# Optimization experiments

Hardware: AMD Instinct MI355X
Metric: run time of the kernel (lower is better)

Reference implementation:

```python
import jax, jax.numpy as jnp
import numpy as np

N = 100000   # nodes
G = 128      # graphs for mean pool


def gcn_conv(x, edge_index, W, b, num_nodes):
    # PyG GCNConv (default): x' = D^-1/2 (A+I) D^-1/2 (x W) + b
    x = x @ W
    src, dst = edge_index[0], edge_index[1]
    loop = jnp.arange(num_nodes)
    src = jnp.concatenate([src, loop])
    dst = jnp.concatenate([dst, loop])
    ones = jnp.ones(src.shape[0], x.dtype)
    deg = jax.ops.segment_sum(ones, dst, num_segments=num_nodes)
    dinv = jnp.where(deg > 0, jax.lax.rsqrt(deg), 0.0)
    norm = dinv[src] * dinv[dst]            # [E+N]
    msg = x[src] * norm[:, None]            # gather + scale
    out = jax.ops.segment_sum(msg, dst, num_segments=num_nodes)  # scatter-add
    return out + b


def setup_inputs() -> dict:
    key = jax.random.key(0)
    ks = jax.random.split(key, 5)
    x = jax.random.normal(ks[0], (N, 128), jnp.float32)
    edge_index = jax.random.randint(ks[1], (2, 1600000), 0, N)
    batch = jnp.sort(jax.random.randint(ks[2], (N,), 0, G))
    W1 = jax.random.normal(ks[3], (128, 64), jnp.float32) / np.sqrt(128.0)
    b1 = jnp.zeros((64,), jnp.float32)
    W2 = jax.random.normal(ks[4], (64, 64), jnp.float32) / np.sqrt(64.0)
    b2 = jnp.zeros((64,), jnp.float32)
    return {"x": x, "edge_index": edge_index, "batch": batch,
            "W1": W1, "b1": b1, "W2": W2, "b2": b2}


def reference(x, edge_index, batch, W1, b1, W2, b2):
    h = gcn_conv(x, edge_index, W1, b1, N)
    h = jax.nn.relu(h)  # dropout is identity in eval mode
    h = gcn_conv(h, edge_index, W2, b2, N)
    # global_mean_pool over graph ids
    s = jax.ops.segment_sum(h, batch, num_segments=G)
    cnt = jax.ops.segment_sum(jnp.ones((N,), h.dtype), batch, num_segments=G)
    return s / jnp.maximum(cnt, 1.0)[:, None]   # [G, hidden2]
```

## Files before the change

kernel.cpp:

```cpp
#include <hip/hip_runtime.h>
#include <hip/hip_fp16.h>

#define SLOTS 64
#define DEGSTRIDE 16

typedef _Float16 half8 __attribute__((ext_vector_type(8)));
typedef float f32x4 __attribute__((ext_vector_type(4)));

__global__ __launch_bounds__(256) void fused_fill_gemm(
    const int* __restrict__ src, const int* __restrict__ dst, int E, int N,
    int* __restrict__ degp, int* __restrict__ colpad, int chunks,
    const float* __restrict__ in, const float* __restrict__ W,
    __half* __restrict__ out, int tiles) {
  constexpr int K = 128;
  constexpr int LDK = K + 8;
  __shared__ __align__(16) _Float16 Wt[64][LDK];
  int bid = blockIdx.x;

  if (bid < 8 * chunks) {
    int range = bid & 7;
    int chunk = bid >> 3;
    int per = (N + 7) >> 3;
    int lo = range * per, hi = min(N, lo + per);
    int e0 = (int)((long long)chunk * E / chunks);
    int e1 = (int)((long long)(chunk + 1) * E / chunks);
    for (int e = e0 + (int)threadIdx.x; e < e1; e += 256) {
      int d = dst[e];
      if (d >= lo && d < hi) {
        int p = atomicAdd(&degp[(size_t)d * DEGSTRIDE], 1);
        if (p < SLOTS) colpad[(size_t)d * SLOTS + p] = src[e];
      }
    }
    return;
  }

  int tile = bid - 8 * chunks;
  if (tile >= tiles) return;
  int t = threadIdx.x;
  int wave = t >> 6, lane = t & 63;
  int arow = lane & 15, kgrp = lane >> 4;
  constexpr int KK = K / 32;
  int row0 = tile * 64;
  int row = row0 + wave * 16 + arow;

  half8 af[KK];
  if (row < N) {
#pragma unroll
    for (int kk = 0; kk < KK; ++kk) {
      const float4* p = (const float4*)&in[(size_t)row * K + kk * 32 + kgrp * 8];
      float4 v0 = p[0], v1 = p[1];
      half8 h;
      h[0] = (_Float16)v0.x; h[1] = (_Float16)v0.y;
      h[2] = (_Float16)v0.z; h[3] = (_Float16)v0.w;
      h[4] = (_Float16)v1.x; h[5] = (_Float16)v1.y;
      h[6] = (_Float16)v1.z; h[7] = (_Float16)v1.w;
      af[kk] = h;
    }
  } else {
#pragma unroll
    for (int kk = 0; kk < KK; ++kk) af[kk] = (half8)((_Float16)0.f);
  }

  for (int j = t; j < K * 64; j += 256) {
    int k = j >> 6, c = j & 63;
    Wt[c][k] = (_Float16)W[j];
  }
  __syncthreads();

  f32x4 acc[4];
#pragma unroll
  for (int ct = 0; ct < 4; ++ct) acc[ct] = (f32x4)(0.f);
#pragma unroll
  for (int kk = 0; kk < KK; ++kk) {
#pragma unroll
    for (int ct = 0; ct < 4; ++ct) {
      half8 b = *(const half8*)&Wt[ct * 16 + arow][kk * 32 + kgrp * 8];
      acc[ct] = __builtin_amdgcn_mfma_f32_16x16x32_f16(af[kk], b, acc[ct], 0, 0, 0);
    }
  }

  int rbase = row0 + wave * 16 + kgrp * 4;
#pragma unroll
  for (int r = 0; r < 4; ++r) {
    int rr = rbase + r;
    if (rr < N) {
#pragma unroll
      for (int ct = 0; ct < 4; ++ct)
        out[(size_t)rr * 64 + ct * 16 + arow] = __float2half(acc[ct][r]);
    }
  }
}

__global__ __launch_bounds__(256) void scale_dinv(const int* __restrict__ degp,
                                                  __half* __restrict__ g,
                                                  float* __restrict__ dinv,
                                                  int* __restrict__ degc, int N) {
  int idx = blockIdx.x * 256 + threadIdx.x;
  if (idx >= N * 8) return;
  int row = idx >> 3;
  int d = degp[(size_t)row * DEGSTRIDE];
  float s = rsqrtf((float)(d + 1));
  half8 h = *(half8*)&g[(size_t)idx * 8];
#pragma unroll
  for (int j = 0; j < 8; ++j) h[j] = (_Float16)((float)h[j] * s);
  *(half8*)&g[(size_t)idx * 8] = h;
  if ((idx & 7) == 0) {
    dinv[row] = s;
    degc[row] = min(d, SLOTS);
  }
}

__global__ __launch_bounds__(256) void gemm_mfma64(const __half* __restrict__ in,
                                                   const float* __restrict__ W,
                                                   const float* __restrict__ dinv,
                                                   __half* __restrict__ out, int N) {
  constexpr int K = 64;
  constexpr int LDK = K + 8;
  __shared__ __align__(16) _Float16 Wt[64][LDK];
  int t = threadIdx.x;
  int wave = t >> 6, lane = t & 63;
  int arow = lane & 15, kgrp = lane >> 4;
  constexpr int KK = K / 32;
  int row0 = blockIdx.x * 64;
  int row = row0 + wave * 16 + arow;

  half8 af[KK];
  if (row < N) {
#pragma unroll
    for (int kk = 0; kk < KK; ++kk)
      af[kk] = *(const half8*)&in[(size_t)row * K + kk * 32 + kgrp * 8];
  } else {
#pragma unroll
    for (int kk = 0; kk < KK; ++kk) af[kk] = (half8)((_Float16)0.f);
  }
  int rbase = row0 + wave * 16 + kgrp * 4;
  float dv[4];
#pragma unroll
  for (int r = 0; r < 4; ++r) dv[r] = (rbase + r < N) ? dinv[rbase + r] : 0.f;

  for (int j = t; j < K * 64; j += 256) {
    int k = j >> 6, c = j & 63;
    Wt[c][k] = (_Float16)W[j];
  }
  __syncthreads();

  f32x4 acc[4];
#pragma unroll
  for (int ct = 0; ct < 4; ++ct) acc[ct] = (f32x4)(0.f);
#pragma unroll
  for (int kk = 0; kk < KK; ++kk) {
#pragma unroll
    for (int ct = 0; ct < 4; ++ct) {
      half8 b = *(const half8*)&Wt[ct * 16 + arow][kk * 32 + kgrp * 8];
      acc[ct] = __builtin_amdgcn_mfma_f32_16x16x32_f16(af[kk], b, acc[ct], 0, 0, 0);
    }
  }
#pragma unroll
  for (int r = 0; r < 4; ++r) {
    int rr = rbase + r;
    if (rr < N) {
#pragma unroll
      for (int ct = 0; ct < 4; ++ct)
        out[(size_t)rr * 64 + ct * 16 + arow] = __float2half(acc[ct][r] * dv[r]);
    }
  }
}

__global__ __launch_bounds__(256) void aggregate(const __half* __restrict__ g,
                                                 const int* __restrict__ degc,
                                                 const int* __restrict__ colpad,
                                                 const float* __restrict__ dinv,
                                                 const float* __restrict__ bias,
                                                 const int* __restrict__ batch,
                                                 __half* __restrict__ out,
                                                 float* __restrict__ poolsum,
                                                 float* __restrict__ poolcnt,
                                                 int N, int mode) {
  int lane = threadIdx.x & 63;
  int wave = blockIdx.x * 4 + (threadIdx.x >> 6);
  int nwaves = gridDim.x * 4;
  int per = (N + nwaves - 1) / nwaves;
  int n0 = wave * per, n1 = min(N, n0 + per);
  if (n0 >= n1) return;
  float b = bias[lane];
  int cur = mode ? batch[n0] : 0;
  float pacc = 0.f, pcnt = 0.f;
  int deg = degc[n0];
  int nb = colpad[(size_t)n0 * SLOTS + lane];
  for (int node = n0; node < n1; ++node) {
    int nxt = (node + 1 < n1) ? node + 1 : node;
    int dn = degc[nxt];
    int nbn = colpad[(size_t)nxt * SLOTS + lane];
    float a0 = __half2float(g[(size_t)node * 64 + lane]);
    float a1 = 0.f, a2 = 0.f, a3 = 0.f;
    float a4 = 0.f, a5 = 0.f, a6 = 0.f, a7 = 0.f;
    int j = 0;
    for (; j + 7 < deg; j += 8) {
      int s0 = __shfl(nb, j, 64);
      int s1 = __shfl(nb, j + 1, 64);
      int s2 = __shfl(nb, j + 2, 64);
      int s3 = __shfl(nb, j + 3, 64);
      int s4 = __shfl(nb, j + 4, 64);
      int s5 = __shfl(nb, j + 5, 64);
      int s6 = __shfl(nb, j + 6, 64);
      int s7 = __shfl(nb, j + 7, 64);
      a0 += __half2float(g[(size_t)s0 * 64 + lane]);
      a1 += __half2float(g[(size_t)s1 * 64 + lane]);
      a2 += __half2float(g[(size_t)s2 * 64 + lane]);
      a3 += __half2float(g[(size_t)s3 * 64 + lane]);
      a4 += __half2float(g[(size_t)s4 * 64 + lane]);
      a5 += __half2float(g[(size_t)s5 * 64 + lane]);
      a6 += __half2float(g[(size_t)s6 * 64 + lane]);
      a7 += __half2float(g[(size_t)s7 * 64 + lane]);
    }
    for (; j + 3 < deg; j += 4) {
      int s0 = __shfl(nb, j, 64);
      int s1 = __shfl(nb, j + 1, 64);
      int s2 = __shfl(nb, j + 2, 64);
      int s3 = __shfl(nb, j + 3, 64);
      a0 += __half2float(g[(size_t)s0 * 64 + lane]);
      a1 += __half2float(g[(size_t)s1 * 64 + lane]);
      a2 += __half2float(g[(size_t)s2 * 64 + lane]);
      a3 += __half2float(g[(size_t)s3 * 64 + lane]);
    }
    for (; j < deg; ++j) a0 += __half2float(g[(size_t)__shfl(nb, j, 64) * 64 + lane]);
    float r = dinv[node] * (((a0 + a1) + (a2 + a3)) + ((a4 + a5) + (a6 + a7))) + b;
    deg = dn;
    nb = nbn;
    if (mode == 0) {
      out[(size_t)node * 64 + lane] = __float2half(fmaxf(r, 0.f));
    } else {
      int bg = batch[node];
      if (bg != cur) {
        atomicAdd(&poolsum[cur * 64 + lane], pacc);
        if (lane == 0) atomicAdd(&poolcnt[cur], pcnt);
        pacc = 0.f; pcnt = 0.f; cur = bg;
      }
      pacc += r; pcnt += 1.f;
    }
  }
  if (mode) {
    atomicAdd(&poolsum[cur * 64 + lane], pacc);
    if (lane == 0) atomicAdd(&poolcnt[cur], pcnt);
  }
}

__global__ __launch_bounds__(256) void finalize(const float* __restrict__ poolsum,
                                                const float* __restrict__ poolcnt,
                                                float* __restrict__ out, int Gn) {
  int i = blockIdx.x * 256 + threadIdx.x;
  if (i < Gn * 64) {
    float c = poolcnt[i >> 6];
    out[i] = poolsum[i] / fmaxf(c, 1.f);
  }
}

extern "C" void kernel_launch(void* const* d_in, const int* in_sizes, int n_in,
                              void* d_out, int out_size, void* d_ws, size_t ws_size,
                              hipStream_t stream) {
  const float* x   = (const float*)d_in[0];
  const int* ei    = (const int*)d_in[1];
  const int* batch = (const int*)d_in[2];
  const float* W1  = (const float*)d_in[3];
  const float* b1  = (const float*)d_in[4];
  const float* W2  = (const float*)d_in[5];
  const float* b2  = (const float*)d_in[6];
  float* out = (float*)d_out;

  int N  = in_sizes[2];
  int E  = in_sizes[1] / 2;
  int Gn = out_size / 64;

  char* ws = (char*)d_ws;
  size_t off = 0;
  auto alloc = [&](size_t bytes) -> void* {
    void* p = ws + off;
    off = (off + bytes + 255) & ~(size_t)255;
    return p;
  };
  float* poolsum = (float*)alloc(4ull * Gn * 64);
  float* poolcnt = (float*)alloc(4ull * Gn);
  size_t zero_bytes = off;
  int* colpad    = (int*)alloc(4ull * (size_t)N * SLOTS);
  float* dinv    = (float*)alloc(4ull * N);
  int* degc      = (int*)alloc(4ull * N);
  __half* gbuf   = (__half*)alloc(2ull * (size_t)N * 64);
  __half* ybuf   = (__half*)alloc(2ull * (size_t)N * 64);
  int* degp = (int*)ybuf;
  (void)ws_size; (void)n_in;

  hipMemsetAsync(poolsum, 0, zero_bytes, stream);
  hipMemsetAsync(degp, 0, 4ull * (size_t)N * DEGSTRIDE, stream);

  const int* srcv = ei;
  const int* dstv = ei + E;
  int tiles64 = (N + 63) / 64;
  int chunks = 256;

  fused_fill_gemm<<<8 * chunks + tiles64, 256, 0, stream>>>(
      srcv, dstv, E, N, degp, colpad, chunks, x, W1, gbuf, tiles64);
  scale_dinv<<<(N * 8 + 255) / 256, 256, 0, stream>>>(degp, gbuf, dinv, degc, N);

  aggregate<<<2048, 256, 0, stream>>>(gbuf, degc, colpad, dinv, b1, batch, ybuf,
                                      nullptr, nullptr, N, 0);
  gemm_mfma64<<<tiles64, 256, 0, stream>>>(ybuf, W2, dinv, gbuf, N);
  aggregate<<<2048, 256, 0, stream>>>(gbuf, degc, colpad, dinv, b2, batch, nullptr,
                                      poolsum, poolcnt, N, 1);
  finalize<<<(Gn * 64 + 255) / 256, 256, 0, stream>>>(poolsum, poolcnt, out, Gn);
}
```

Before: 308.3 us.

## Commute second-layer GEMM past aggregation and pooling into finalize

Uses linearity to move the second layer's W2 multiply after mean pooling: layer 1 now writes dinv-prescaled relu output, layer-2 aggregation sums raw features, and a small finalize kernel applies W2 and b2 to the pooled means. This removes the full N x 64 x 64 GEMM kernel and its extra round trip through memory. The neighbour-index loads are also masked to the valid degree, which cuts unneeded colpad reads. The risk is a change in rounding, since fp16 features are aggregated before the projection, and the bias is skipped for empty graphs.

Result: faster. 300.7 us (-2.4%).

```diff
diff --git a/kernel.cpp b/kernel.cpp
--- a/kernel.cpp
+++ b/kernel.cpp
@@ -107,62 +107,6 @@
   if ((idx & 7) == 0) {
     dinv[row] = s;
     degc[row] = min(d, SLOTS);
-  }
-}
-
-__global__ __launch_bounds__(256) void gemm_mfma64(const __half* __restrict__ in,
-                                                   const float* __restrict__ W,
-                                                   const float* __restrict__ dinv,
-                                                   __half* __restrict__ out, int N) {
-  constexpr int K = 64;
-  constexpr int LDK = K + 8;
-  __shared__ __align__(16) _Float16 Wt[64][LDK];
-  int t = threadIdx.x;
-  int wave = t >> 6, lane = t & 63;
-  int arow = lane & 15, kgrp = lane >> 4;
-  constexpr int KK = K / 32;
-  int row0 = blockIdx.x * 64;
-  int row = row0 + wave * 16 + arow;
-
-  half8 af[KK];
-  if (row < N) {
-#pragma unroll
-    for (int kk = 0; kk < KK; ++kk)
-      af[kk] = *(const half8*)&in[(size_t)row * K + kk * 32 + kgrp * 8];
-  } else {
-#pragma unroll
-    for (int kk = 0; kk < KK; ++kk) af[kk] = (half8)((_Float16)0.f);
-  }
-  int rbase = row0 + wave * 16 + kgrp * 4;
-  float dv[4];
-#pragma unroll
-  for (int r = 0; r < 4; ++r) dv[r] = (rbase + r < N) ? dinv[rbase + r] : 0.f;
-
-  for (int j = t; j < K * 64; j += 256) {
-    int k = j >> 6, c = j & 63;
-    Wt[c][k] = (_Float16)W[j];
-  }
-  __syncthreads();
-
-  f32x4 acc[4];
-#pragma unroll
-  for (int ct = 0; ct < 4; ++ct) acc[ct] = (f32x4)(0.f);
-#pragma unroll
-  for (int kk = 0; kk < KK; ++kk) {
-#pragma unroll
-    for (int ct = 0; ct < 4; ++ct) {
-      half8 b = *(const half8*)&Wt[ct * 16 + arow][kk * 32 + kgrp * 8];
-      acc[ct] = __builtin_amdgcn_mfma_f32_16x16x32_f16(af[kk], b, acc[ct], 0, 0, 0);
-    }
-  }
-#pragma unroll
-  for (int r = 0; r < 4; ++r) {
-    int rr = rbase + r;
-    if (rr < N) {
-#pragma unroll
-      for (int ct = 0; ct < 4; ++ct)
-        out[(size_t)rr * 64 + ct * 16 + arow] = __float2half(acc[ct][r] * dv[r]);
-    }
   }
 }
 
@@ -182,15 +126,15 @@
   int per = (N + nwaves - 1) / nwaves;
   int n0 = wave * per, n1 = min(N, n0 + per);
   if (n0 >= n1) return;
-  float b = bias[lane];
+  float b = (mode == 0) ? bias[lane] : 0.f;
   int cur = mode ? batch[n0] : 0;
   float pacc = 0.f, pcnt = 0.f;
   int deg = degc[n0];
-  int nb = colpad[(size_t)n0 * SLOTS + lane];
+  int nb = (lane < deg) ? colpad[(size_t)n0 * SLOTS + lane] : 0;
   for (int node = n0; node < n1; ++node) {
     int nxt = (node + 1 < n1) ? node + 1 : node;
     int dn = degc[nxt];
-    int nbn = colpad[(size_t)nxt * SLOTS + lane];
+    int nbn = (lane < dn) ? colpad[(size_t)nxt * SLOTS + lane] : 0;
     float a0 = __half2float(g[(size_t)node * 64 + lane]);
     float a1 = 0.f, a2 = 0.f, a3 = 0.f;
     float a4 = 0.f, a5 = 0.f, a6 = 0.f, a7 = 0.f;
@@ -224,11 +168,12 @@
       a3 += __half2float(g[(size_t)s3 * 64 + lane]);
     }
     for (; j < deg; ++j) a0 += __half2float(g[(size_t)__shfl(nb, j, 64) * 64 + lane]);
-    float r = dinv[node] * (((a0 + a1) + (a2 + a3)) + ((a4 + a5) + (a6 + a7))) + b;
+    float dnode = dinv[node];
+    float r = dnode * (((a0 + a1) + (a2 + a3)) + ((a4 + a5) + (a6 + a7))) + b;
     deg = dn;
     nb = nbn;
     if (mode == 0) {
-      out[(size_t)node * 64 + lane] = __float2half(fmaxf(r, 0.f));
+      out[(size_t)node * 64 + lane] = __float2half(dnode * fmaxf(r, 0.f));
     } else {
       int bg = batch[node];
       if (bg != cur) {
@@ -245,14 +190,21 @@
   }
 }
 
-__global__ __launch_bounds__(256) void finalize(const float* __restrict__ poolsum,
-                                                const float* __restrict__ poolcnt,
-                                                float* __restrict__ out, int Gn) {
-  int i = blockIdx.x * 256 + threadIdx.x;
-  if (i < Gn * 64) {
-    float c = poolcnt[i >> 6];
-    out[i] = poolsum[i] / fmaxf(c, 1.f);
-  }
+__global__ __launch_bounds__(64) void finalize_gemm(const float* __restrict__ poolsum,
+                                                    const float* __restrict__ poolcnt,
+                                                    const float* __restrict__ W2,
+                                                    const float* __restrict__ b2,
+                                                    float* __restrict__ out, int Gn) {
+  __shared__ float m[64];
+  int g = blockIdx.x, c = threadIdx.x;
+  float cnt = poolcnt[g];
+  float inv = (cnt > 0.f) ? 1.f / cnt : 0.f;
+  m[c] = poolsum[g * 64 + c] * inv;
+  __syncthreads();
+  float acc = 0.f;
+#pragma unroll
+  for (int k = 0; k < 64; ++k) acc = fmaf(m[k], W2[k * 64 + c], acc);
+  out[g * 64 + c] = (cnt > 0.f) ? acc + b2[c] : 0.f;
 }
 
 extern "C" void kernel_launch(void* const* d_in, const int* in_sizes, int n_in,
@@ -303,8 +255,7 @@
 
   aggregate<<<2048, 256, 0, stream>>>(gbuf, degc, colpad, dinv, b1, batch, ybuf,
                                       nullptr, nullptr, N, 0);
-  gemm_mfma64<<<tiles64, 256, 0, stream>>>(ybuf, W2, dinv, gbuf, N);
-  aggregate<<<2048, 256, 0, stream>>>(gbuf, degc, colpad, dinv, b2, batch, nullptr,
+  aggregate<<<2048, 256, 0, stream>>>(ybuf, degc, colpad, dinv, b1, batch, nullptr,
                                       poolsum, poolcnt, N, 1);
-  finalize<<<(Gn * 64 + 255) / 256, 256, 0, stream>>>(poolsum, poolcnt, out, Gn);
-}
+  finalize_gemm<<<Gn, 64, 0, stream>>>(poolsum, poolcnt, W2, b2, out, Gn);
+}
```
